# Kernel tuning notes

Measured on AMD Instinct MI355X. Metric: run time of the kernel, lower is better.

## Reference

```python
import jax, jax.numpy as jnp
import numpy as np

B, D_ENC, T = 4, 512, 256
D_PRED, U = 640, 128
H, V = 640, 1025  # joint_hidden, num_classes + blank


def setup_inputs() -> dict:
    key = jax.random.key(0)
    ks = jax.random.split(key, 8)
    s = lambda d: 1.0 / np.sqrt(d)
    return {
        "encoder_outputs": jax.random.normal(ks[0], (B, D_ENC, T), jnp.float32),
        "decoder_outputs": jax.random.normal(ks[1], (B, D_PRED, U), jnp.float32),
        "W_enc": jax.random.normal(ks[2], (H, D_ENC), jnp.float32) * s(D_ENC),
        "b_enc": jax.random.normal(ks[3], (H,), jnp.float32) * s(D_ENC),
        "W_pred": jax.random.normal(ks[4], (H, D_PRED), jnp.float32) * s(D_PRED),
        "b_pred": jax.random.normal(ks[5], (H,), jnp.float32) * s(D_PRED),
        "W_out": jax.random.normal(ks[6], (V, H), jnp.float32) * s(H),
        "b_out": jax.random.normal(ks[7], (H,), jnp.float32)[:0],  # placeholder, replaced below
    } | {"b_out": jax.random.normal(jax.random.fold_in(key, 99), (V,), jnp.float32) * s(H)}


def reference(encoder_outputs, decoder_outputs, W_enc, b_enc, W_pred, b_pred, W_out, b_out):
    # transpose to (B, T, D_enc) and (B, U, D_pred)
    enc = jnp.swapaxes(encoder_outputs, 1, 2)
    dec = jnp.swapaxes(decoder_outputs, 1, 2)
    # projections to joint hidden
    f = jnp.einsum('bte,he->bth', enc, W_enc) + b_enc   # [B,T,H]
    g = jnp.einsum('bup,hp->buh', dec, W_pred) + b_pred  # [B,U,H]
    # broadcast add -> [B,T,U,H], ReLU, output linear, log-softmax
    h = jax.nn.relu(f[:, :, None, :] + g[:, None, :, :])
    logits = jnp.einsum('btuh,vh->btuv', h, W_out) + b_out  # [B,T,U,V]
    return jax.nn.log_softmax(logits, axis=-1)
```

## Files before the change

kernel.cpp:

```cpp
#include <hip/hip_runtime.h>
#include <hip/hip_bf16.h>

#define NB 4
#define NT 256
#define NU 128
#define DENC 512
#define DPRED 640
#define NH 640
#define NV 1025
#define NVP 1152
#define NTILES 72
#define JT 18
#define KSTEPS 20
#define WSLAB (NVP * 32)

typedef __attribute__((ext_vector_type(8))) short short8;
typedef __attribute__((ext_vector_type(4))) float f32x4;

__device__ __forceinline__ unsigned short bfu(float a) {
    union { __hip_bfloat16 h; unsigned short u; } cv;
    cv.h = __float2bfloat16(a);
    return cv.u;
}

__device__ __forceinline__ unsigned pk2(float a, float b) {
    union { __hip_bfloat162 h; unsigned u; } cv;
    cv.h = __float22bfloat162_rn(float2{a, b});
    return cv.u;
}

__device__ __forceinline__ short8 pack_relu(f32x4 x, f32x4 y) {
    union { short8 s; unsigned u[4]; } r;
    r.u[0] = pk2(fmaxf(x[0], 0.f), fmaxf(x[1], 0.f));
    r.u[1] = pk2(fmaxf(x[2], 0.f), fmaxf(x[3], 0.f));
    r.u[2] = pk2(fmaxf(y[0], 0.f), fmaxf(y[1], 0.f));
    r.u[3] = pk2(fmaxf(y[2], 0.f), fmaxf(y[3], 0.f));
    return r.s;
}

__device__ __forceinline__ void gload_lds16(const void* g, void* l) {
    __builtin_amdgcn_global_load_lds(
        (const __attribute__((address_space(1))) unsigned int*)g,
        (__attribute__((address_space(3))) unsigned int*)l, 16, 0, 0);
}

__global__ __launch_bounds__(256) void prep_kernel(const float* __restrict__ Wo,
                                                   const float* __restrict__ bo,
                                                   unsigned short* __restrict__ WbT,
                                                   float* __restrict__ biasp) {
    int idx = blockIdx.x * 256 + threadIdx.x;
    int ks = blockIdx.y;
    int r = idx >> 5;
    int kk = idx & 31;
    int s = kk >> 3, e = kk & 7;
    int f = ((r >> 2) ^ r) & 3;
    int scol = ks * 32 + (((s ^ f) & 3) << 3) + e;
    WbT[(size_t)ks * WSLAB + idx] = (r < NV) ? bfu(Wo[r * NH + scol]) : (unsigned short)0;
    if (ks == 0 && idx < NVP) biasp[idx] = (idx < NV) ? bo[idx] : -1e30f;
}

__global__ __launch_bounds__(256) void proj_kernel(const float* __restrict__ X,
                                                   const float* __restrict__ W,
                                                   const float* __restrict__ bias,
                                                   float* __restrict__ out,
                                                   int L, int K) {
    __shared__ unsigned short As[32][40];
    __shared__ unsigned short Bs[64][40];
    int tid = threadIdx.x;
    int wave = tid >> 6, lane = tid & 63;
    int col16 = lane & 15, kgrp = lane >> 4;
    int m0 = blockIdx.x * 32;
    int n0 = blockIdx.y * 64;
    int b = m0 / L, l0 = m0 % L;
    const float* Xb = X + (size_t)b * K * L;

    float bv = bias[n0 + wave * 16 + col16];
    f32x4 c0 = {bv, bv, bv, bv};
    f32x4 c1 = c0;

    int ac = tid >> 3;
    int ar = (tid & 7) * 4;
    int bn = tid >> 2;
    int bc = (tid & 3) * 8;

    for (int k0 = 0; k0 < K; k0 += 32) {
        f32x4 av  = *(const f32x4*)(Xb + (size_t)(k0 + ac) * L + l0 + ar);
        f32x4 bw0 = *(const f32x4*)(W + (size_t)(n0 + bn) * K + k0 + bc);
        f32x4 bw1 = *(const f32x4*)(W + (size_t)(n0 + bn) * K + k0 + bc + 4);
        __syncthreads();
        As[ar + 0][ac] = bfu(av[0]);
        As[ar + 1][ac] = bfu(av[1]);
        As[ar + 2][ac] = bfu(av[2]);
        As[ar + 3][ac] = bfu(av[3]);
        unsigned* bsrow = (unsigned*)&Bs[bn][bc];
        bsrow[0] = pk2(bw0[0], bw0[1]);
        bsrow[1] = pk2(bw0[2], bw0[3]);
        bsrow[2] = pk2(bw1[0], bw1[1]);
        bsrow[3] = pk2(bw1[2], bw1[3]);
        __syncthreads();
        short8 a0  = *(const short8*)&As[col16][kgrp * 8];
        short8 a1  = *(const short8*)&As[16 + col16][kgrp * 8];
        short8 bfr = *(const short8*)&Bs[wave * 16 + col16][kgrp * 8];
        c0 = __builtin_amdgcn_mfma_f32_16x16x32_bf16(a0, bfr, c0, 0, 0, 0);
        c1 = __builtin_amdgcn_mfma_f32_16x16x32_bf16(a1, bfr, c1, 0, 0, 0);
    }
    int n = n0 + wave * 16 + col16;
    #pragma unroll
    for (int i = 0; i < 4; ++i) {
        int r0 = kgrp * 4 + i;
        out[(size_t)(m0 + r0) * NH + n]      = c0[i];
        out[(size_t)(m0 + 16 + r0) * NH + n] = c1[i];
    }
}

__global__ __launch_bounds__(256, 2) void joint_kernel(const float* __restrict__ f,
                                                       const float* __restrict__ g,
                                                       const unsigned short* __restrict__ WbT,
                                                       const float* __restrict__ biasp,
                                                       float* __restrict__ out) {
    __shared__ unsigned short Ws[WSLAB];
    __shared__ float fs[NH];
    __shared__ float redm[4][32];
    __shared__ float reds[4][32];
    int tid = threadIdx.x;
    int wave = tid >> 6, lane = tid & 63;
    int col16 = lane & 15, kgrp = lane >> 4;
    int bt = blockIdx.x >> 2;
    int u0 = (blockIdx.x & 3) * 32;
    int b = bt >> 8;

    for (int i = tid; i < NH; i += 256) fs[i] = f[(size_t)bt * NH + i];

    int tA = wave * 9;
    int tB = 36 + wave * 9;

    const float* gp[2];
    #pragma unroll
    for (int m = 0; m < 2; ++m)
        gp[m] = g + (size_t)(b * NU + u0 + m * 16 + col16) * NH + kgrp * 8;

    f32x4 c[JT][2];
    #pragma unroll
    for (int j = 0; j < JT; ++j) {
        int tile = (j < 9) ? (tA + j) : (tB + j - 9);
        float bv = biasp[tile * 16 + col16];
        f32x4 cv = {bv, bv, bv, bv};
        c[j][0] = cv; c[j][1] = cv;
    }

    #pragma unroll
    for (int jj = 0; jj < 9; ++jj)
        gload_lds16(WbT + (size_t)(tA + jj) * 512 + lane * 8, &Ws[(tA + jj) * 512]);
    #pragma unroll
    for (int jj = 0; jj < 9; ++jj)
        gload_lds16(WbT + (size_t)(tB + jj) * 512 + lane * 8, &Ws[(tB + jj) * 512]);

    f32x4 gpre[2][2];
    #pragma unroll
    for (int m = 0; m < 2; ++m) {
        gpre[m][0] = *(const f32x4*)(gp[m]);
        gpre[m][1] = *(const f32x4*)(gp[m] + 4);
    }

    int slx = ((kgrp ^ ((col16 >> 2) ^ col16)) & 3) * 8;
    int rdbase = col16 * 32 + slx;

    __syncthreads();

    for (int ks = 0; ks < KSTEPS; ++ks) {
        int kb = ks * 32 + kgrp * 8;
        f32x4 fa0 = *(const f32x4*)(fs + kb);
        f32x4 fa1 = *(const f32x4*)(fs + kb + 4);
        short8 a0 = pack_relu(fa0 + gpre[0][0], fa1 + gpre[0][1]);
        short8 a1 = pack_relu(fa0 + gpre[1][0], fa1 + gpre[1][1]);
        if (ks < KSTEPS - 1) {
            gpre[0][0] = *(const f32x4*)(gp[0] + (ks + 1) * 32);
            gpre[0][1] = *(const f32x4*)(gp[0] + (ks + 1) * 32 + 4);
            gpre[1][0] = *(const f32x4*)(gp[1] + (ks + 1) * 32);
            gpre[1][1] = *(const f32x4*)(gp[1] + (ks + 1) * 32 + 4);
        }
        __builtin_amdgcn_s_setprio(1);
        #pragma unroll
        for (int jj = 0; jj < 9; ++jj) {
            short8 bj = *(const short8*)&Ws[(tA + jj) * 512 + rdbase];
            c[jj][0] = __builtin_amdgcn_mfma_f32_16x16x32_bf16(a0, bj, c[jj][0], 0, 0, 0);
            c[jj][1] = __builtin_amdgcn_mfma_f32_16x16x32_bf16(a1, bj, c[jj][1], 0, 0, 0);
        }
        __builtin_amdgcn_s_setprio(0);
        __syncthreads();
        if (ks < KSTEPS - 1) {
            const unsigned short* wn = WbT + (size_t)(ks + 1) * WSLAB;
            #pragma unroll
            for (int jj = 0; jj < 9; ++jj)
                gload_lds16(wn + (size_t)(tA + jj) * 512 + lane * 8, &Ws[(tA + jj) * 512]);
        }
        __builtin_amdgcn_s_setprio(1);
        #pragma unroll
        for (int jj = 0; jj < 9; ++jj) {
            short8 bj = *(const short8*)&Ws[(tB + jj) * 512 + rdbase];
            c[9 + jj][0] = __builtin_amdgcn_mfma_f32_16x16x32_bf16(a0, bj, c[9 + jj][0], 0, 0, 0);
            c[9 + jj][1] = __builtin_amdgcn_mfma_f32_16x16x32_bf16(a1, bj, c[9 + jj][1], 0, 0, 0);
        }
        __builtin_amdgcn_s_setprio(0);
        __syncthreads();
        if (ks < KSTEPS - 1) {
            const unsigned short* wn = WbT + (size_t)(ks + 1) * WSLAB;
            #pragma unroll
            for (int jj = 0; jj < 9; ++jj)
                gload_lds16(wn + (size_t)(tB + jj) * 512 + lane * 8, &Ws[(tB + jj) * 512]);
        }
    }

    float mx[2][4], sl[2][4];
    #pragma unroll
    for (int m = 0; m < 2; ++m) {
        #pragma unroll
        for (int i = 0; i < 4; ++i) {
            float v = -3e38f;
            #pragma unroll
            for (int j = 0; j < JT; ++j) v = fmaxf(v, c[j][m][i]);
            #pragma unroll
            for (int d = 1; d < 16; d <<= 1)
                v = fmaxf(v, __shfl_xor(v, d, 64));
            mx[m][i] = v;
        }
    }
    if (col16 == 0) {
        #pragma unroll
        for (int m = 0; m < 2; ++m)
            #pragma unroll
            for (int i = 0; i < 4; ++i)
                redm[wave][m * 16 + kgrp * 4 + i] = mx[m][i];
    }
    __syncthreads();
    #pragma unroll
    for (int m = 0; m < 2; ++m)
        #pragma unroll
        for (int i = 0; i < 4; ++i) {
            int r = m * 16 + kgrp * 4 + i;
            mx[m][i] = fmaxf(fmaxf(redm[0][r], redm[1][r]), fmaxf(redm[2][r], redm[3][r]));
        }
    #pragma unroll
    for (int m = 0; m < 2; ++m) {
        #pragma unroll
        for (int i = 0; i < 4; ++i) {
            float ssum = 0.f;
            #pragma unroll
            for (int j = 0; j < JT; ++j) ssum += __expf(c[j][m][i] - mx[m][i]);
            #pragma unroll
            for (int d = 1; d < 16; d <<= 1)
                ssum += __shfl_xor(ssum, d, 64);
            sl[m][i] = ssum;
        }
    }
    if (col16 == 0) {
        #pragma unroll
        for (int m = 0; m < 2; ++m)
            #pragma unroll
            for (int i = 0; i < 4; ++i)
                reds[wave][m * 16 + kgrp * 4 + i] = sl[m][i];
    }
    __syncthreads();
    #pragma unroll
    for (int m = 0; m < 2; ++m)
        #pragma unroll
        for (int i = 0; i < 4; ++i) {
            int r = m * 16 + kgrp * 4 + i;
            float S = (reds[0][r] + reds[1][r]) + (reds[2][r] + reds[3][r]);
            sl[m][i] = mx[m][i] + __logf(S);
        }

    size_t orow0 = (size_t)bt * NU + u0;
    #pragma unroll
    for (int m = 0; m < 2; ++m) {
        #pragma unroll
        for (int j = 0; j < JT; ++j) {
            int tile = (j < 9) ? (tA + j) : (tB + j - 9);
            int col = tile * 16 + col16;
            if (col < NV) {
                #pragma unroll
                for (int i = 0; i < 4; ++i) {
                    size_t row = orow0 + m * 16 + kgrp * 4 + i;
                    out[row * (size_t)NV + col] = c[j][m][i] - sl[m][i];
                }
            }
        }
    }
}

extern "C" void kernel_launch(void* const* d_in, const int* in_sizes, int n_in,
                              void* d_out, int out_size, void* d_ws, size_t ws_size,
                              hipStream_t stream) {
    const float* enc    = (const float*)d_in[0];
    const float* dec    = (const float*)d_in[1];
    const float* W_enc  = (const float*)d_in[2];
    const float* b_enc  = (const float*)d_in[3];
    const float* W_pred = (const float*)d_in[4];
    const float* b_pred = (const float*)d_in[5];
    const float* W_out  = (const float*)d_in[6];
    const float* b_out  = (const float*)d_in[7];
    float* out = (float*)d_out;

    char* ws = (char*)d_ws;
    unsigned short* WbT = (unsigned short*)ws;
    float* biasp = (float*)(ws + 1474560);
    float* fbuf  = (float*)(ws + 1479168);
    float* gbuf  = (float*)(ws + 4100608);

    prep_kernel<<<dim3(WSLAB / 256, KSTEPS), 256, 0, stream>>>(W_out, b_out, WbT, biasp);
    proj_kernel<<<dim3((NB * NT) / 32, NH / 64), 256, 0, stream>>>(enc, W_enc, b_enc, fbuf, NT, DENC);
    proj_kernel<<<dim3((NB * NU) / 32, NH / 64), 256, 0, stream>>>(dec, W_pred, b_pred, gbuf, NU, DPRED);
    joint_kernel<<<NB * NT * (NU / 32), 256, 0, stream>>>(fbuf, gbuf, WbT, biasp, out);
}
```

Baseline: 1.003 ms.

## Pad vocab to 68 tiles and replace block barriers with per-wave waitcnt pipelining

The output vocabulary padding shrinks from 72 to 68 tiles, and each wave now owns a contiguous run of 17 tiles (split 8+9), so it only reads LDS slabs it loaded itself. The per-stage __syncthreads calls are replaced by explicit s_waitcnt vmcnt/lgkmcnt counts and sched barriers, letting waves run their load/compute pipeline independently. An extra zero slab is written by prep so the final prefetch stays in bounds, and the g loads become unconditional. This cuts padded MFMA work and barrier stalls, but the results depend on hand-tuned vmcnt counts matching the compiler's instruction order.

```diff
diff --git a/kernel.cpp b/kernel.cpp
--- a/kernel.cpp
+++ b/kernel.cpp
@@ -8,9 +8,11 @@
 #define DPRED 640
 #define NH 640
 #define NV 1025
-#define NVP 1152
-#define NTILES 72
-#define JT 18
+#define NVP 1088
+#define NTILES 68
+#define JTA 8
+#define JTB 9
+#define JT 17
 #define KSTEPS 20
 #define WSLAB (NVP * 32)
 
@@ -55,7 +57,9 @@
     int s = kk >> 3, e = kk & 7;
     int f = ((r >> 2) ^ r) & 3;
     int scol = ks * 32 + (((s ^ f) & 3) << 3) + e;
-    WbT[(size_t)ks * WSLAB + idx] = (r < NV) ? bfu(Wo[r * NH + scol]) : (unsigned short)0;
+    unsigned short val = 0;
+    if (ks < KSTEPS && r < NV) val = bfu(Wo[r * NH + scol]);
+    WbT[(size_t)ks * WSLAB + idx] = val;
     if (ks == 0 && idx < NVP) biasp[idx] = (idx < NV) ? bo[idx] : -1e30f;
 }
 
@@ -131,85 +135,81 @@
 
     for (int i = tid; i < NH; i += 256) fs[i] = f[(size_t)bt * NH + i];
 
-    int tA = wave * 9;
-    int tB = 36 + wave * 9;
-
-    const float* gp[2];
-    #pragma unroll
-    for (int m = 0; m < 2; ++m)
-        gp[m] = g + (size_t)(b * NU + u0 + m * 16 + col16) * NH + kgrp * 8;
+    int tstart = wave * JT;
+    unsigned short* WsA = &Ws[tstart * 512];
+    unsigned short* WsB = &Ws[(tstart + JTA) * 512];
+
+    const float* gp0 = g + (size_t)(b * NU + u0 + col16) * NH + kgrp * 8;
+    const float* gp1 = gp0 + 16 * NH;
 
     f32x4 c[JT][2];
     #pragma unroll
     for (int j = 0; j < JT; ++j) {
-        int tile = (j < 9) ? (tA + j) : (tB + j - 9);
-        float bv = biasp[tile * 16 + col16];
+        float bv = biasp[(tstart + j) * 16 + col16];
         f32x4 cv = {bv, bv, bv, bv};
         c[j][0] = cv; c[j][1] = cv;
     }
 
-    #pragma unroll
-    for (int jj = 0; jj < 9; ++jj)
-        gload_lds16(WbT + (size_t)(tA + jj) * 512 + lane * 8, &Ws[(tA + jj) * 512]);
-    #pragma unroll
-    for (int jj = 0; jj < 9; ++jj)
-        gload_lds16(WbT + (size_t)(tB + jj) * 512 + lane * 8, &Ws[(tB + jj) * 512]);
-
-    f32x4 gpre[2][2];
-    #pragma unroll
-    for (int m = 0; m < 2; ++m) {
-        gpre[m][0] = *(const f32x4*)(gp[m]);
-        gpre[m][1] = *(const f32x4*)(gp[m] + 4);
-    }
-
     int slx = ((kgrp ^ ((col16 >> 2) ^ col16)) & 3) * 8;
     int rdbase = col16 * 32 + slx;
 
     __syncthreads();
+
+    f32x4 ga0 = *(const f32x4*)(gp0);
+    f32x4 ga1 = *(const f32x4*)(gp0 + 4);
+    f32x4 gb0 = *(const f32x4*)(gp1);
+    f32x4 gb1 = *(const f32x4*)(gp1 + 4);
+    #pragma unroll
+    for (int jj = 0; jj < JTA; ++jj)
+        gload_lds16(WbT + (size_t)(tstart + jj) * 512 + lane * 8, WsA + jj * 512);
+    #pragma unroll
+    for (int jj = 0; jj < JTB; ++jj)
+        gload_lds16(WbT + (size_t)(tstart + JTA + jj) * 512 + lane * 8, WsB + jj * 512);
 
     for (int ks = 0; ks < KSTEPS; ++ks) {
         int kb = ks * 32 + kgrp * 8;
         f32x4 fa0 = *(const f32x4*)(fs + kb);
         f32x4 fa1 = *(const f32x4*)(fs + kb + 4);
-        short8 a0 = pack_relu(fa0 + gpre[0][0], fa1 + gpre[0][1]);
-        short8 a1 = pack_relu(fa0 + gpre[1][0], fa1 + gpre[1][1]);
-        if (ks < KSTEPS - 1) {
-            gpre[0][0] = *(const f32x4*)(gp[0] + (ks + 1) * 32);
-            gpre[0][1] = *(const f32x4*)(gp[0] + (ks + 1) * 32 + 4);
-            gpre[1][0] = *(const f32x4*)(gp[1] + (ks + 1) * 32);
-            gpre[1][1] = *(const f32x4*)(gp[1] + (ks + 1) * 32 + 4);
-        }
+        short8 a0 = pack_relu(fa0 + ga0, fa1 + ga1);
+        short8 a1 = pack_relu(fa0 + gb0, fa1 + gb1);
+        ga0 = *(const f32x4*)(gp0 + (ks + 1) * 32);
+        ga1 = *(const f32x4*)(gp0 + (ks + 1) * 32 + 4);
+        gb0 = *(const f32x4*)(gp1 + (ks + 1) * 32);
+        gb1 = *(const f32x4*)(gp1 + (ks + 1) * 32 + 4);
+        asm volatile("s_waitcnt vmcnt(13)" ::: "memory");
+        __builtin_amdgcn_sched_barrier(0);
         __builtin_amdgcn_s_setprio(1);
         #pragma unroll
-        for (int jj = 0; jj < 9; ++jj) {
-            short8 bj = *(const short8*)&Ws[(tA + jj) * 512 + rdbase];
+        for (int jj = 0; jj < JTA; ++jj) {
+            short8 bj = *(const short8*)(WsA + jj * 512 + rdbase);
             c[jj][0] = __builtin_amdgcn_mfma_f32_16x16x32_bf16(a0, bj, c[jj][0], 0, 0, 0);
             c[jj][1] = __builtin_amdgcn_mfma_f32_16x16x32_bf16(a1, bj, c[jj][1], 0, 0, 0);
         }
         __builtin_amdgcn_s_setprio(0);
-        __syncthreads();
-        if (ks < KSTEPS - 1) {
-            const unsigned short* wn = WbT + (size_t)(ks + 1) * WSLAB;
-            #pragma unroll
-            for (int jj = 0; jj < 9; ++jj)
-                gload_lds16(wn + (size_t)(tA + jj) * 512 + lane * 8, &Ws[(tA + jj) * 512]);
-        }
+        asm volatile("s_waitcnt lgkmcnt(0)" ::: "memory");
+        __builtin_amdgcn_sched_barrier(0);
+        const unsigned short* wn = WbT + (size_t)(ks + 1) * WSLAB;
+        #pragma unroll
+        for (int jj = 0; jj < JTA; ++jj)
+            gload_lds16(wn + (size_t)(tstart + jj) * 512 + lane * 8, WsA + jj * 512);
+        asm volatile("s_waitcnt vmcnt(12)" ::: "memory");
+        __builtin_amdgcn_sched_barrier(0);
         __builtin_amdgcn_s_setprio(1);
         #pragma unroll
-        for (int jj = 0; jj < 9; ++jj) {
-            short8 bj = *(const short8*)&Ws[(tB + jj) * 512 + rdbase];
-            c[9 + jj][0] = __builtin_amdgcn_mfma_f32_16x16x32_bf16(a0, bj, c[9 + jj][0], 0, 0, 0);
-            c[9 + jj][1] = __builtin_amdgcn_mfma_f32_16x16x32_bf16(a1, bj, c[9 + jj][1], 0, 0, 0);
+        for (int jj = 0; jj < JTB; ++jj) {
+            short8 bj = *(const short8*)(WsB + jj * 512 + rdbase);
+            c[JTA + jj][0] = __builtin_amdgcn_mfma_f32_16x16x32_bf16(a0, bj, c[JTA + jj][0], 0, 0, 0);
+            c[JTA + jj][1] = __builtin_amdgcn_mfma_f32_16x16x32_bf16(a1, bj, c[JTA + jj][1], 0, 0, 0);
         }
         __builtin_amdgcn_s_setprio(0);
-        __syncthreads();
-        if (ks < KSTEPS - 1) {
-            const unsigned short* wn = WbT + (size_t)(ks + 1) * WSLAB;
-            #pragma unroll
-            for (int jj = 0; jj < 9; ++jj)
-                gload_lds16(wn + (size_t)(tB + jj) * 512 + lane * 8, &Ws[(tB + jj) * 512]);
-        }
-    }
+        asm volatile("s_waitcnt lgkmcnt(0)" ::: "memory");
+        __builtin_amdgcn_sched_barrier(0);
+        #pragma unroll
+        for (int jj = 0; jj < JTB; ++jj)
+            gload_lds16(wn + (size_t)(tstart + JTA + jj) * 512 + lane * 8, WsB + jj * 512);
+    }
+
+    __syncthreads();
 
     float mx[2][4], sl[2][4];
     #pragma unroll
@@ -275,8 +275,7 @@
     for (int m = 0; m < 2; ++m) {
         #pragma unroll
         for (int j = 0; j < JT; ++j) {
-            int tile = (j < 9) ? (tA + j) : (tB + j - 9);
-            int col = tile * 16 + col16;
+            int col = (tstart + j) * 16 + col16;
             if (col < NV) {
                 #pragma unroll
                 for (int i = 0; i < 4; ++i) {
@@ -303,11 +302,11 @@
 
     char* ws = (char*)d_ws;
     unsigned short* WbT = (unsigned short*)ws;
-    float* biasp = (float*)(ws + 1474560);
-    float* fbuf  = (float*)(ws + 1479168);
-    float* gbuf  = (float*)(ws + 4100608);
-
-    prep_kernel<<<dim3(WSLAB / 256, KSTEPS), 256, 0, stream>>>(W_out, b_out, WbT, biasp);
+    float* biasp = (float*)(ws + 1462272);
+    float* fbuf  = (float*)(ws + 1466624);
+    float* gbuf  = (float*)(ws + 4088064);
+
+    prep_kernel<<<dim3(WSLAB / 256, KSTEPS + 1), 256, 0, stream>>>(W_out, b_out, WbT, biasp);
     proj_kernel<<<dim3((NB * NT) / 32, NH / 64), 256, 0, stream>>>(enc, W_enc, b_enc, fbuf, NT, DENC);
     proj_kernel<<<dim3((NB * NU) / 32, NH / 64), 256, 0, stream>>>(dec, W_pred, b_pred, gbuf, NU, DPRED);
     joint_kernel<<<NB * NT * (NU / 32), 256, 0, stream>>>(fbuf, gbuf, WbT, biasp, out);
```

After: 903.0 us. -10.0%, faster.
